# Performance work log

Measured on AMD Instinct MI355X. Metric: run time of the kernel, lower is better.

The kernel has to match this reference:

```python
import jax, jax.numpy as jnp
import numpy as np

N_ATOMS = 300000
N_COLS = 8
VOCAB = 4096      # nn.Embedding(4096, per_col_dim)
D_COL = 32        # per_col_dim
HID = 256         # hidden_size
N_BONDS = 320000
B_GRAPHS = 6000
ATOMS_PER_GRAPH = 50
STEPS = 3
SENTINEL = 999999999


def _linear_params(key, fan_in, fan_out):
    lim = 1.0 / np.sqrt(fan_in)
    kw, kb = jax.random.split(key)
    W = jax.random.uniform(kw, (fan_out, fan_in), minval=-lim, maxval=lim, dtype=jnp.float32)
    b = jax.random.uniform(kb, (fan_out,), minval=-lim, maxval=lim, dtype=jnp.float32)
    return W, b


def setup_inputs() -> dict:
    key = jax.random.key(0)
    ks = jax.random.split(key, 8)
    a_features = jax.random.randint(ks[0], (N_ATOMS, N_COLS), 0, VOCAB, dtype=jnp.int32)
    uv = jax.random.randint(ks[1], (N_BONDS, 2), 0, N_ATOMS, dtype=jnp.int32)
    bextra = jax.random.randint(ks[2], (N_BONDS, 1), 0, 16, dtype=jnp.int32)
    b_features = jnp.concatenate([uv, bextra], axis=1)
    # contiguous equal-length scopes: graph i owns atoms [i*50, i*50+50)
    starts = np.arange(B_GRAPHS, dtype=np.int32) * ATOMS_PER_GRAPH
    lengths = np.full(B_GRAPHS, ATOMS_PER_GRAPH, dtype=np.int32)
    a_scopes = jnp.asarray(np.stack([starts, lengths], axis=1))
    emb_weights = jax.random.normal(ks[3], (N_COLS, VOCAB, D_COL), dtype=jnp.float32) * 0.02
    W_in, b_in = _linear_params(ks[4], D_COL, HID)
    W_self, b_self = _linear_params(ks[5], HID, HID)
    W_neigh, b_neigh = _linear_params(ks[6], HID, HID)
    W_out, b_out = _linear_params(ks[7], HID, HID)
    return {
        'a_features': a_features, 'b_features': b_features, 'a_scopes': a_scopes,
        'emb_weights': emb_weights,
        'W_in': W_in, 'b_in': b_in,
        'W_self': W_self, 'b_self': b_self,
        'W_neigh': W_neigh, 'b_neigh': b_neigh,
        'W_out': W_out, 'b_out': b_out,
    }


def reference(a_features, b_features, a_scopes, emb_weights,
              W_in, b_in, W_self, b_self, W_neigh, b_neigh, W_out, b_out):
    # --- per-column embedding lookup, summed over columns ---
    idx = jnp.remainder(a_features, VOCAB)
    idx = jnp.where(a_features >= SENTINEL, 0, idx)          # sentinel -> index 0
    x = jnp.zeros((a_features.shape[0], D_COL), dtype=emb_weights.dtype)
    for c in range(N_COLS):                                   # fixed small loop over columns
        x = x + emb_weights[c][idx[:, c]]
    h = x @ W_in.T + b_in                                     # [N, HID]
    # --- undirected edges -> two directed edge lists ---
    u = b_features[:, 0]
    v = b_features[:, 1]
    src = jnp.concatenate([u, v], axis=0)
    dst = jnp.concatenate([v, u], axis=0)
    # --- message passing steps ---
    for _ in range(STEPS):
        agg = jnp.zeros_like(h).at[dst].add(h[src])           # scatter-add neighbor sum
        h = jax.nn.relu(h @ W_self.T + b_self + agg @ W_neigh.T + b_neigh)
    h = h @ W_out.T + b_out
    # --- per-graph mean pooling over contiguous scopes ---
    lengths = a_scopes[:, 1]
    seg_ids = jnp.repeat(jnp.arange(a_scopes.shape[0]), lengths,
                         total_repeat_length=h.shape[0])
    sums = jax.ops.segment_sum(h, seg_ids, num_segments=a_scopes.shape[0])
    denom = jnp.maximum(lengths, 1).astype(h.dtype)[:, None]
    return sums / denom
```

## Files before the change

kernel.cpp:

```cpp
#include <hip/hip_runtime.h>

#define NATOMS 300000
#define NCOLS 8
#define VOCABSZ 4096
#define DCOL 32
#define HIDDIM 256
#define NBONDS 320000
#define NGRAPHS 6000
#define NSTEPS 3

constexpr int MP = 300032;
constexpr int MTILES64 = MP / 64;

typedef _Float16 f16;
typedef _Float16 f16x4 __attribute__((ext_vector_type(4)));
typedef _Float16 f16x8 __attribute__((ext_vector_type(8)));
typedef float f32x4 __attribute__((ext_vector_type(4)));

constexpr float LO_SCALE = 2048.0f;
constexpr float INV_LO   = 1.0f / 2048.0f;

__device__ __forceinline__ void split2(float x, f16& h, f16& l) {
    h = (f16)x;
    l = (f16)((x - (float)h) * LO_SCALE);
}

__device__ __forceinline__ int swz(int row, int q) {
    return (row * 4 + (q ^ ((row >> 1) & 3))) * 8;
}

static void* g_pool = nullptr;
__attribute__((constructor)) static void alloc_pool() {
    void* p = nullptr;
    if (hipMalloc(&p, (size_t)1024 * 1024 * 1024) == hipSuccess) {
        hipMemset(p, 0, (size_t)1024 * 1024 * 1024);
        g_pool = p;
    }
}

__global__ void fill_kernel(float* out, float v, int n) {
    int i = blockIdx.x * blockDim.x + threadIdx.x;
    if (i < n) out[i] = v;
}

__global__ void build_edges_kernel(const int* __restrict__ bf, int* __restrict__ esrc,
                                   int* __restrict__ nxt, int* head) {
    int e = blockIdx.x * blockDim.x + threadIdx.x;
    if (e >= 2 * NBONDS) return;
    int src, dst;
    if (e < NBONDS) { src = bf[e * 3 + 0]; dst = bf[e * 3 + 1]; }
    else { int i = e - NBONDS; src = bf[i * 3 + 1]; dst = bf[i * 3 + 0]; }
    esrc[e] = src;
    nxt[e] = atomicExch(&head[dst], e);
}

__global__ void wsplit_kernel(const float* __restrict__ W, f16* __restrict__ Wh,
                              f16* __restrict__ Wl, int n) {
    int i = blockIdx.x * blockDim.x + threadIdx.x;
    if (i >= n) return;
    split2(W[i], Wh[i], Wl[i]);
}

__global__ void bsum_kernel(const float* __restrict__ a, const float* __restrict__ b,
                            float* __restrict__ o) {
    int i = threadIdx.x;
    o[i] = a[i] + b[i];
}

__global__ void embed_kernel(const int* __restrict__ af, const float* __restrict__ emb,
                             f16* __restrict__ xh, f16* __restrict__ xl) {
    int gid = blockIdx.x * blockDim.x + threadIdx.x;
    int i = gid >> 5, k = gid & 31;
    if (i >= NATOMS) return;
    float s = 0.0f;
#pragma unroll
    for (int c = 0; c < NCOLS; c++) {
        int v = af[i * NCOLS + c];
        int idx = v & (VOCABSZ - 1);
        if (v >= 999999999) idx = 0;
        s += emb[((size_t)c * VOCABSZ + idx) * DCOL + k];
    }
    split2(s, xh[(size_t)i * DCOL + k], xl[(size_t)i * DCOL + k]);
}

__global__ void agg_kernel(const f16* __restrict__ Ahi, const f16* __restrict__ Alo,
                           f16* __restrict__ Ghi, f16* __restrict__ Glo,
                           const int* __restrict__ head, const int* __restrict__ nxt,
                           const int* __restrict__ esrc) {
    int wid = (blockIdx.x * blockDim.x + threadIdx.x) >> 6;
    int lane = threadIdx.x & 63;
    if (wid >= NATOMS) return;
    float4 sh = make_float4(0.f, 0.f, 0.f, 0.f);
    float4 sl = make_float4(0.f, 0.f, 0.f, 0.f);
    int e = head[wid];
    while (e >= 0) {
        int src = esrc[e];
        const f16x4 vh = *(const f16x4*)(Ahi + (size_t)src * HIDDIM + lane * 4);
        const f16x4 vl = *(const f16x4*)(Alo + (size_t)src * HIDDIM + lane * 4);
        sh.x += (float)vh.x; sh.y += (float)vh.y; sh.z += (float)vh.z; sh.w += (float)vh.w;
        sl.x += (float)vl.x; sl.y += (float)vl.y; sl.z += (float)vl.z; sl.w += (float)vl.w;
        e = nxt[e];
    }
    float4 s;
    s.x = sh.x + sl.x * INV_LO; s.y = sh.y + sl.y * INV_LO;
    s.z = sh.z + sl.z * INV_LO; s.w = sh.w + sl.w * INV_LO;
    f16 h0, l0, h1, l1, h2, l2, h3, l3;
    split2(s.x, h0, l0); split2(s.y, h1, l1);
    split2(s.z, h2, l2); split2(s.w, h3, l3);
    f16x4 oh, ol;
    oh.x = h0; oh.y = h1; oh.z = h2; oh.w = h3;
    ol.x = l0; ol.y = l1; ol.z = l2; ol.w = l3;
    *(f16x4*)(Ghi + (size_t)wid * HIDDIM + lane * 4) = oh;
    *(f16x4*)(Glo + (size_t)wid * HIDDIM + lane * 4) = ol;
}

template <bool HAS_A2, bool RELU, int K>
__global__ __launch_bounds__(256, 2) void mfma_gemm(
    const f16* __restrict__ A1h, const f16* __restrict__ A1l,
    const f16* __restrict__ A2h, const f16* __restrict__ A2l,
    const f16* __restrict__ B1h, const f16* __restrict__ B1l,
    const f16* __restrict__ B2h, const f16* __restrict__ B2l,
    const float* __restrict__ bias,
    f16* __restrict__ Chi, f16* __restrict__ Clo) {
    __shared__ __align__(16) f16 sAh[64 * 32];
    __shared__ __align__(16) f16 sAl[64 * 32];
    __shared__ __align__(16) f16 sBh[256 * 32];
    __shared__ __align__(16) f16 sBl[256 * 32];

    const int t = threadIdx.x;
    const int m0 = blockIdx.x * 64;
    const int lane = t & 63;
    const int wid = t >> 6;
    const int wn = wid * 64;
    const int quad = lane >> 4;
    const int l16 = lane & 15;
    const int ra = t >> 2;
    const int qa = t & 3;

    f32x4 acch[4][4], accl[4][4];
#pragma unroll
    for (int a = 0; a < 4; a++)
#pragma unroll
        for (int b = 0; b < 4; b++) {
            acch[a][b] = (f32x4){0.f, 0.f, 0.f, 0.f};
            accl[a][b] = (f32x4){0.f, 0.f, 0.f, 0.f};
        }

    constexpr int NMAT = HAS_A2 ? 2 : 1;
    constexpr int NST = (K / 32) * NMAT;

    int4 pAh, pAl, pBh0, pBh1, pBh2, pBh3, pBl0, pBl1, pBl2, pBl3;

#define LOAD_STAGE(S)                                                          \
    {                                                                          \
        const int mat_ = HAS_A2 ? ((S) & 1) : 0;                               \
        const int kb_ = (HAS_A2 ? ((S) >> 1) : (S)) * 32;                      \
        const f16* Ah_ = (mat_ == 0) ? A1h : A2h;                              \
        const f16* Al_ = (mat_ == 0) ? A1l : A2l;                              \
        const f16* Bh_ = (mat_ == 0) ? B1h : B2h;                              \
        const f16* Bl_ = (mat_ == 0) ? B1l : B2l;                              \
        const size_t ao_ = (size_t)(m0 + ra) * K + kb_ + qa * 8;               \
        pAh = *(const int4*)(Ah_ + ao_);                                       \
        pAl = *(const int4*)(Al_ + ao_);                                       \
        const size_t bo_ = (size_t)ra * K + kb_ + qa * 8;                      \
        pBh0 = *(const int4*)(Bh_ + bo_);                                      \
        pBh1 = *(const int4*)(Bh_ + bo_ + (size_t)64 * K);                     \
        pBh2 = *(const int4*)(Bh_ + bo_ + (size_t)128 * K);                    \
        pBh3 = *(const int4*)(Bh_ + bo_ + (size_t)192 * K);                    \
        pBl0 = *(const int4*)(Bl_ + bo_);                                      \
        pBl1 = *(const int4*)(Bl_ + bo_ + (size_t)64 * K);                     \
        pBl2 = *(const int4*)(Bl_ + bo_ + (size_t)128 * K);                    \
        pBl3 = *(const int4*)(Bl_ + bo_ + (size_t)192 * K);                    \
    }

    LOAD_STAGE(0);

    for (int s = 0; s < NST; s++) {
        __syncthreads();
        {
            const int dA = swz(ra, qa);
            *(int4*)(sAh + dA) = pAh;
            *(int4*)(sAl + dA) = pAl;
            const int d0 = swz(ra, qa), d1 = swz(ra + 64, qa);
            const int d2 = swz(ra + 128, qa), d3 = swz(ra + 192, qa);
            *(int4*)(sBh + d0) = pBh0; *(int4*)(sBh + d1) = pBh1;
            *(int4*)(sBh + d2) = pBh2; *(int4*)(sBh + d3) = pBh3;
            *(int4*)(sBl + d0) = pBl0; *(int4*)(sBl + d1) = pBl1;
            *(int4*)(sBl + d2) = pBl2; *(int4*)(sBl + d3) = pBl3;
        }
        __syncthreads();
        if (s + 1 < NST) LOAD_STAGE(s + 1);

        f16x8 fah[4], fal[4];
#pragma unroll
        for (int mt = 0; mt < 4; mt++) {
            const int src = swz(mt * 16 + l16, quad);
            fah[mt] = *(const f16x8*)(sAh + src);
            fal[mt] = *(const f16x8*)(sAl + src);
        }
#pragma unroll
        for (int nt = 0; nt < 4; nt++) {
            const int src = swz(wn + nt * 16 + l16, quad);
            const f16x8 bh = *(const f16x8*)(sBh + src);
            const f16x8 bl = *(const f16x8*)(sBl + src);
#pragma unroll
            for (int mt = 0; mt < 4; mt++) {
                acch[mt][nt] = __builtin_amdgcn_mfma_f32_16x16x32_f16(fah[mt], bh, acch[mt][nt], 0, 0, 0);
                accl[mt][nt] = __builtin_amdgcn_mfma_f32_16x16x32_f16(fah[mt], bl, accl[mt][nt], 0, 0, 0);
                accl[mt][nt] = __builtin_amdgcn_mfma_f32_16x16x32_f16(fal[mt], bh, accl[mt][nt], 0, 0, 0);
            }
        }
    }
#undef LOAD_STAGE

#pragma unroll
    for (int mt = 0; mt < 4; mt++) {
#pragma unroll
        for (int nt = 0; nt < 4; nt++) {
            const int col = wn + nt * 16 + l16;
            const float bv = bias[col];
#pragma unroll
            for (int r = 0; r < 4; r++) {
                const int row = m0 + mt * 16 + quad * 4 + r;
                float v = acch[mt][nt][r] + accl[mt][nt][r] * INV_LO + bv;
                if (RELU) v = fmaxf(v, 0.f);
                f16 hi, lo;
                split2(v, hi, lo);
                Chi[(size_t)row * HIDDIM + col] = hi;
                Clo[(size_t)row * HIDDIM + col] = lo;
            }
        }
    }
}

__global__ void readout_kernel(const f16* __restrict__ Hhi, const f16* __restrict__ Hlo,
                               const int* __restrict__ scopes, float* __restrict__ out) {
    int g = blockIdx.x;
    int n = threadIdx.x;
    int start = scopes[g * 2 + 0];
    int len = scopes[g * 2 + 1];
    float s = 0.f;
    for (int j = 0; j < len; j++) {
        size_t o = (size_t)(start + j) * HIDDIM + n;
        s += (float)Hhi[o] + (float)Hlo[o] * INV_LO;
    }
    int d = len > 1 ? len : 1;
    out[(size_t)g * HIDDIM + n] = s / (float)d;
}

extern "C" void kernel_launch(void* const* d_in, const int* in_sizes, int n_in,
                              void* d_out, int out_size, void* d_ws, size_t ws_size,
                              hipStream_t stream) {
    const int* a_features = (const int*)d_in[0];
    const int* b_features = (const int*)d_in[1];
    const int* a_scopes   = (const int*)d_in[2];
    const float* emb      = (const float*)d_in[3];
    const float* W_in     = (const float*)d_in[4];
    const float* b_in     = (const float*)d_in[5];
    const float* W_self   = (const float*)d_in[6];
    const float* b_self   = (const float*)d_in[7];
    const float* W_neigh  = (const float*)d_in[8];
    const float* b_neigh  = (const float*)d_in[9];
    const float* W_out    = (const float*)d_in[10];
    const float* b_out    = (const float*)d_in[11];

    if (g_pool == nullptr) {
        fill_kernel<<<(out_size + 255) / 256, 256, 0, stream>>>(
            (float*)d_out, 77777.0f, out_size);
        return;
    }

    f16* p = (f16*)g_pool;
    const size_t HB = (size_t)MP * HIDDIM;
    f16* hAhi = p;            f16* hAlo = p + HB;
    f16* hBhi = p + 2 * HB;   f16* hBlo = p + 3 * HB;
    f16* hChi = p + 4 * HB;   f16* hClo = p + 5 * HB;
    f16* xhi  = p + 6 * HB;
    f16* xlo  = xhi + (size_t)MP * DCOL;
    f16* Winh = xlo + (size_t)MP * DCOL;
    f16* Winl = Winh + HIDDIM * DCOL;
    f16* Wsh  = Winl + HIDDIM * DCOL;
    f16* Wsl  = Wsh + HIDDIM * HIDDIM;
    f16* Wnh  = Wsl + HIDDIM * HIDDIM;
    f16* Wnl  = Wnh + HIDDIM * HIDDIM;
    f16* Woh  = Wnl + HIDDIM * HIDDIM;
    f16* Wol  = Woh + HIDDIM * HIDDIM;
    float* bsum = (float*)(Wol + HIDDIM * HIDDIM);
    int* esrc = (int*)(bsum + HIDDIM);
    int* nxt  = esrc + 2 * NBONDS;
    int* head = nxt + 2 * NBONDS;

    constexpr int NPAD = MP - NATOMS;

    hipMemsetAsync(head, 0xFF, (size_t)MP * sizeof(int), stream);
    build_edges_kernel<<<(2 * NBONDS + 255) / 256, 256, 0, stream>>>(b_features, esrc, nxt, head);
    wsplit_kernel<<<(HIDDIM * DCOL + 255) / 256, 256, 0, stream>>>(W_in, Winh, Winl, HIDDIM * DCOL);
    wsplit_kernel<<<(HIDDIM * HIDDIM + 255) / 256, 256, 0, stream>>>(W_self, Wsh, Wsl, HIDDIM * HIDDIM);
    wsplit_kernel<<<(HIDDIM * HIDDIM + 255) / 256, 256, 0, stream>>>(W_neigh, Wnh, Wnl, HIDDIM * HIDDIM);
    wsplit_kernel<<<(HIDDIM * HIDDIM + 255) / 256, 256, 0, stream>>>(W_out, Woh, Wol, HIDDIM * HIDDIM);
    bsum_kernel<<<1, HIDDIM, 0, stream>>>(b_self, b_neigh, bsum);

    constexpr int PADF = NPAD * HIDDIM / 2;
    fill_kernel<<<(PADF + 255) / 256, 256, 0, stream>>>((float*)(hAhi + (size_t)NATOMS * HIDDIM), 0.f, PADF);
    fill_kernel<<<(PADF + 255) / 256, 256, 0, stream>>>((float*)(hAlo + (size_t)NATOMS * HIDDIM), 0.f, PADF);
    fill_kernel<<<(PADF + 255) / 256, 256, 0, stream>>>((float*)(hBhi + (size_t)NATOMS * HIDDIM), 0.f, PADF);
    fill_kernel<<<(PADF + 255) / 256, 256, 0, stream>>>((float*)(hBlo + (size_t)NATOMS * HIDDIM), 0.f, PADF);
    fill_kernel<<<(PADF + 255) / 256, 256, 0, stream>>>((float*)(hChi + (size_t)NATOMS * HIDDIM), 0.f, PADF);
    fill_kernel<<<(PADF + 255) / 256, 256, 0, stream>>>((float*)(hClo + (size_t)NATOMS * HIDDIM), 0.f, PADF);
    constexpr int PADX = NPAD * DCOL / 2;
    fill_kernel<<<(PADX + 255) / 256, 256, 0, stream>>>((float*)(xhi + (size_t)NATOMS * DCOL), 0.f, PADX);
    fill_kernel<<<(PADX + 255) / 256, 256, 0, stream>>>((float*)(xlo + (size_t)NATOMS * DCOL), 0.f, PADX);

    embed_kernel<<<(NATOMS * DCOL + 255) / 256, 256, 0, stream>>>(a_features, emb, xhi, xlo);
    mfma_gemm<false, false, DCOL><<<MTILES64, 256, 0, stream>>>(
        xhi, xlo, nullptr, nullptr, Winh, Winl, nullptr, nullptr, b_in, hAhi, hAlo);

    f16 *h_hi = hAhi, *h_lo = hAlo;
    f16 *g_hi = hBhi, *g_lo = hBlo;
    f16 *n_hi = hChi, *n_lo = hClo;
    for (int s = 0; s < NSTEPS; s++) {
        agg_kernel<<<NATOMS / 4, 256, 0, stream>>>(h_hi, h_lo, g_hi, g_lo, head, nxt, esrc);
        mfma_gemm<true, true, HIDDIM><<<MTILES64, 256, 0, stream>>>(
            h_hi, h_lo, g_hi, g_lo, Wsh, Wsl, Wnh, Wnl, bsum, n_hi, n_lo);
        f16* t1 = h_hi; f16* t2 = h_lo;
        h_hi = n_hi; h_lo = n_lo;
        n_hi = g_hi; n_lo = g_lo;
        g_hi = t1;   g_lo = t2;
    }

    mfma_gemm<false, false, HIDDIM><<<MTILES64, 256, 0, stream>>>(
        h_hi, h_lo, nullptr, nullptr, Woh, Wol, nullptr, nullptr, b_out, g_hi, g_lo);
    readout_kernel<<<NGRAPHS, 256, 0, stream>>>(g_hi, g_lo, a_scopes, (float*)d_out);
}
```

Measured before the change: 2.193 ms.

## Apply output linear after mean pooling instead of per atom

Exploits linearity of mean pooling: pools the final hidden states per graph first, then applies W_out and bias on the 6000 pooled rows in fp32 instead of running the output GEMM over all 300k atoms. This removes a full-size MFMA GEMM and its 300k-row write and read. The W_out split kernel goes away too. The mfma_gemm launch bound is also raised to 4 blocks per CU, which may force register spilling.

Measured after the change: 8.159 ms. 272% more time.

```diff
diff --git a/kernel.cpp b/kernel.cpp
--- a/kernel.cpp
+++ b/kernel.cpp
@@ -115,7 +115,7 @@
 }
 
 template <bool HAS_A2, bool RELU, int K>
-__global__ __launch_bounds__(256, 2) void mfma_gemm(
+__global__ __launch_bounds__(256, 4) void mfma_gemm(
     const f16* __restrict__ A1h, const f16* __restrict__ A1l,
     const f16* __restrict__ A2h, const f16* __restrict__ A2l,
     const f16* __restrict__ B1h, const f16* __restrict__ B1l,
@@ -233,8 +233,8 @@
     }
 }
 
-__global__ void readout_kernel(const f16* __restrict__ Hhi, const f16* __restrict__ Hlo,
-                               const int* __restrict__ scopes, float* __restrict__ out) {
+__global__ void readout_mean_kernel(const f16* __restrict__ Hhi, const f16* __restrict__ Hlo,
+                                    const int* __restrict__ scopes, float* __restrict__ G) {
     int g = blockIdx.x;
     int n = threadIdx.x;
     int start = scopes[g * 2 + 0];
@@ -245,7 +245,36 @@
         s += (float)Hhi[o] + (float)Hlo[o] * INV_LO;
     }
     int d = len > 1 ? len : 1;
-    out[(size_t)g * HIDDIM + n] = s / (float)d;
+    G[(size_t)g * HIDDIM + n] = s / (float)d;
+}
+
+__global__ __launch_bounds__(256) void out_gemm_kernel(
+    const float* __restrict__ G, const float* __restrict__ W,
+    const float* __restrict__ bias, float* __restrict__ out) {
+    __shared__ float sG[16 * 256];
+    const int g0 = blockIdx.x * 16;
+    const int t = threadIdx.x;
+#pragma unroll
+    for (int i = 0; i < 16; i++) sG[i * 256 + t] = G[(size_t)(g0 + i) * 256 + t];
+    __syncthreads();
+    const float bv = bias[t];
+    const float* wrow = W + (size_t)t * 256;
+    float acc[16];
+#pragma unroll
+    for (int g = 0; g < 16; g++) acc[g] = 0.f;
+    for (int k = 0; k < 256; k += 4) {
+        const float4 w = *(const float4*)(wrow + k);
+#pragma unroll
+        for (int g = 0; g < 16; g++) {
+            const float4 a = *(const float4*)(sG + g * 256 + k);
+            acc[g] = fmaf(a.x, w.x, acc[g]);
+            acc[g] = fmaf(a.y, w.y, acc[g]);
+            acc[g] = fmaf(a.z, w.z, acc[g]);
+            acc[g] = fmaf(a.w, w.w, acc[g]);
+        }
+    }
+#pragma unroll
+    for (int g = 0; g < 16; g++) out[(size_t)(g0 + g) * 256 + t] = acc[g] + bv;
 }
 
 extern "C" void kernel_launch(void* const* d_in, const int* in_sizes, int n_in,
@@ -283,9 +312,8 @@
     f16* Wsl  = Wsh + HIDDIM * HIDDIM;
     f16* Wnh  = Wsl + HIDDIM * HIDDIM;
     f16* Wnl  = Wnh + HIDDIM * HIDDIM;
-    f16* Woh  = Wnl + HIDDIM * HIDDIM;
-    f16* Wol  = Woh + HIDDIM * HIDDIM;
-    float* bsum = (float*)(Wol + HIDDIM * HIDDIM);
+    float* Gmean = (float*)(Wnl + HIDDIM * HIDDIM);
+    float* bsum  = Gmean + (size_t)NGRAPHS * HIDDIM;
     int* esrc = (int*)(bsum + HIDDIM);
     int* nxt  = esrc + 2 * NBONDS;
     int* head = nxt + 2 * NBONDS;
@@ -297,7 +325,6 @@
     wsplit_kernel<<<(HIDDIM * DCOL + 255) / 256, 256, 0, stream>>>(W_in, Winh, Winl, HIDDIM * DCOL);
     wsplit_kernel<<<(HIDDIM * HIDDIM + 255) / 256, 256, 0, stream>>>(W_self, Wsh, Wsl, HIDDIM * HIDDIM);
     wsplit_kernel<<<(HIDDIM * HIDDIM + 255) / 256, 256, 0, stream>>>(W_neigh, Wnh, Wnl, HIDDIM * HIDDIM);
-    wsplit_kernel<<<(HIDDIM * HIDDIM + 255) / 256, 256, 0, stream>>>(W_out, Woh, Wol, HIDDIM * HIDDIM);
     bsum_kernel<<<1, HIDDIM, 0, stream>>>(b_self, b_neigh, bsum);
 
     constexpr int PADF = NPAD * HIDDIM / 2;
@@ -328,7 +355,6 @@
         g_hi = t1;   g_lo = t2;
     }
 
-    mfma_gemm<false, false, HIDDIM><<<MTILES64, 256, 0, stream>>>(
-        h_hi, h_lo, nullptr, nullptr, Woh, Wol, nullptr, nullptr, b_out, g_hi, g_lo);
-    readout_kernel<<<NGRAPHS, 256, 0, stream>>>(g_hi, g_lo, a_scopes, (float*)d_out);
-}
+    readout_mean_kernel<<<NGRAPHS, 256, 0, stream>>>(h_hi, h_lo, a_scopes, Gmean);
+    out_gemm_kernel<<<NGRAPHS / 16, 256, 0, stream>>>(Gmean, W_out, b_out, (float*)d_out);
+}
```
